# Kernel optimization log

Measured on AMD Instinct MI355X. Metric: run time of the kernel, lower is better.

The kernel has to match this reference:

```python
import jax, jax.numpy as jnp
import numpy as np

B, T, U, D, INNER, VOCAB = 4, 256, 64, 512, 512, 2048

def setup_inputs() -> dict:
    key = jax.random.key(0)
    ks = jax.random.split(key, 6)
    return {
        "enc_state": jax.random.normal(ks[0], (B, T, D), jnp.float32),
        "dec_state": jax.random.normal(ks[1], (B, U, D), jnp.float32),
        "W1": jax.random.normal(ks[2], (2 * D, INNER), jnp.float32) * 0.02,
        "b1": jax.random.normal(ks[3], (INNER,), jnp.float32) * 0.02,
        "W2": jax.random.normal(ks[4], (INNER, VOCAB), jnp.float32) * 0.02,
        "b2": jax.random.normal(ks[5], (VOCAB,), jnp.float32) * 0.02,
    }

def reference(enc_state, dec_state, W1, b1, W2, b2):
    # concat([enc, dec]) @ W1 == enc @ W1[:D] + dec @ W1[D:]  (same math,
    # avoids materializing the [B,T,U,2D] repeat+cat tensor)
    d = enc_state.shape[-1]
    We, Wd = W1[:d], W1[d:]
    enc_proj = jnp.einsum('btd,dk->btk', enc_state, We)           # [B,T,INNER]
    dec_proj = jnp.einsum('bud,dk->buk', dec_state, Wd)           # [B,U,INNER]
    hidden = jnp.tanh(enc_proj[:, :, None, :] + dec_proj[:, None, :, :] + b1)  # [B,T,U,INNER]
    logits = jnp.einsum('btuk,kv->btuv', hidden, W2) + b2          # [B,T,U,VOCAB]
    return logits
```

## Files before the change

### kernel.cpp

```cpp
#include <hip/hip_runtime.h>
#include <hip/hip_bf16.h>

#define B_  4
#define T_  256
#define U_  64
#define D_  512
#define INNER_ 512
#define VOCAB_ 2048

typedef __attribute__((ext_vector_type(8))) short short8;
typedef __attribute__((ext_vector_type(4))) float f32x4;

__global__ __launch_bounds__(256) void proj_kernel(
    const float* __restrict__ enc, const float* __restrict__ dec,
    const float* __restrict__ W1, const float* __restrict__ b1,
    float* __restrict__ encP, float* __restrict__ decPb) {
  int ct = blockIdx.x;
  int rt = blockIdx.y;
  const float* src; float* dst; int kOff; int addB1; int rowBase;
  if (rt < 64) { src = enc; dst = encP; kOff = 0; addB1 = 0; rowBase = rt * 16; }
  else { src = dec; dst = decPb; kOff = D_; addB1 = 1; rowBase = (rt - 64) * 16; }

  __shared__ float As[16][D_];
  int tid = threadIdx.x;
  const float4* s4 = (const float4*)(src + (size_t)rowBase * D_);
  float4* a4 = (float4*)(&As[0][0]);
#pragma unroll
  for (int i = 0; i < 8; i++) a4[tid + 256 * i] = s4[tid + 256 * i];
  __syncthreads();

  int colQ = (tid & 31) * 4;
  int col = ct * 128 + colQ;
  int r0 = (tid >> 5) * 2;
  float a00=0,a01=0,a02=0,a03=0, a10=0,a11=0,a12=0,a13=0;
  const float* Wp = W1 + (size_t)kOff * INNER_ + col;
#pragma unroll 4
  for (int k = 0; k < D_; k++) {
    float4 w = *(const float4*)(Wp + (size_t)k * INNER_);
    float e0 = As[r0][k], e1 = As[r0 + 1][k];
    a00 += e0 * w.x; a01 += e0 * w.y; a02 += e0 * w.z; a03 += e0 * w.w;
    a10 += e1 * w.x; a11 += e1 * w.y; a12 += e1 * w.z; a13 += e1 * w.w;
  }
  float4 bb = {0,0,0,0};
  if (addB1) bb = *(const float4*)(b1 + col);
  float4 o0 = {a00 + bb.x, a01 + bb.y, a02 + bb.z, a03 + bb.w};
  float4 o1 = {a10 + bb.x, a11 + bb.y, a12 + bb.z, a13 + bb.w};
  *(float4*)(dst + (size_t)(rowBase + r0) * INNER_ + col) = o0;
  *(float4*)(dst + (size_t)(rowBase + r0 + 1) * INNER_ + col) = o1;
}

__global__ __launch_bounds__(256) void w2t_kernel(
    const float* __restrict__ W2, __hip_bfloat16* __restrict__ W2T) {
  __shared__ float tile[32][33];
  int vBase = blockIdx.x * 32;
  int kBase = blockIdx.y * 32;
  int tx = threadIdx.x & 31, ty = threadIdx.x >> 5;
#pragma unroll
  for (int i = 0; i < 32; i += 8)
    tile[ty + i][tx] = W2[(size_t)(kBase + ty + i) * VOCAB_ + vBase + tx];
  __syncthreads();
#pragma unroll
  for (int i = 0; i < 32; i += 8)
    W2T[(size_t)(vBase + ty + i) * INNER_ + kBase + tx] = __float2bfloat16(tile[tx][ty + i]);
}

__global__ __launch_bounds__(256) void hidden_kernel(
    const float* __restrict__ encP, const float* __restrict__ decPb,
    __hip_bfloat16* __restrict__ H) {
  int gid = blockIdx.x * 256 + threadIdx.x;
  int k0 = (gid & 63) * 8;
  int r = gid >> 6;
  int u = r & 63;
  int bt = r >> 6;
  int b = bt >> 8;
  const float4* e = (const float4*)(encP + (size_t)bt * 512 + k0);
  const float4* dv = (const float4*)(decPb + (size_t)(b * 64 + u) * 512 + k0);
  float4 e0 = e[0], e1 = e[1];
  float4 d0 = dv[0], d1 = dv[1];
  union { __hip_bfloat16 h[8]; uint4 v; } p;
  p.h[0] = __float2bfloat16(tanhf(e0.x + d0.x));
  p.h[1] = __float2bfloat16(tanhf(e0.y + d0.y));
  p.h[2] = __float2bfloat16(tanhf(e0.z + d0.z));
  p.h[3] = __float2bfloat16(tanhf(e0.w + d0.w));
  p.h[4] = __float2bfloat16(tanhf(e1.x + d1.x));
  p.h[5] = __float2bfloat16(tanhf(e1.y + d1.y));
  p.h[6] = __float2bfloat16(tanhf(e1.z + d1.z));
  p.h[7] = __float2bfloat16(tanhf(e1.w + d1.w));
  *(uint4*)((__hip_bfloat16*)H + (size_t)r * 512 + k0) = p.v;
}

__device__ inline void gload_lds16(const void* g, void* l) {
  __builtin_amdgcn_global_load_lds(
      (const __attribute__((address_space(1))) unsigned int*)g,
      (__attribute__((address_space(3))) unsigned int*)l, 16, 0, 0);
}

__global__ __launch_bounds__(256, 2) void joint_gemm(
    const __hip_bfloat16* __restrict__ H, const __hip_bfloat16* __restrict__ W2T,
    const float* __restrict__ b2, float* __restrict__ out) {
  extern __shared__ char smem[];
  int tid = threadIdx.x;
  int lane = tid & 63, wave = tid >> 6;
  int wm = wave >> 1, wn = wave & 1;

  int bid = blockIdx.x;
  int wg = (bid & 7) * 512 + (bid >> 3);
  int rt = wg >> 4;
  int ct = wg & 15;
  size_t rowBase = (size_t)rt * 256;
  int colBase = ct * 128;

  int srow = tid >> 2;
  int kswz = ((tid & 3) ^ ((tid >> 3) & 3)) * 8;
  const __hip_bfloat16* pA = H   + (rowBase + srow) * 512 + kswz;
  const __hip_bfloat16* pB = W2T + (size_t)(colBase + srow) * 512 + kswz;
  char* ldsA = smem;
  char* ldsB = smem + 32768;

#define STAGE(t, buf) do {                                                    \
    const __hip_bfloat16* ga = pA + (size_t)(t) * 32;                         \
    const __hip_bfloat16* gb = pB + (size_t)(t) * 32;                         \
    char* la = ldsA + (buf) * 16384 + wave * 1024;                            \
    char* lb = ldsB + (buf) * 8192 + wave * 1024;                             \
    _Pragma("unroll")                                                         \
    for (int j = 0; j < 4; j++)                                               \
      gload_lds16(ga + (size_t)j * 64 * 512, la + j * 4096);                  \
    _Pragma("unroll")                                                         \
    for (int j = 0; j < 2; j++)                                               \
      gload_lds16(gb + (size_t)j * 64 * 512, lb + j * 4096);                  \
  } while (0)

  int laneOff = (lane & 15) * 64 + (((lane >> 4) ^ (((lane & 15) >> 1) & 3)) * 16);
  int offA = wm * 8192 + laneOff;
  int offB = wn * 4096 + laneOff;

  float bv[4];
#pragma unroll
  for (int ni = 0; ni < 4; ni++) bv[ni] = b2[colBase + wn * 64 + ni * 16 + (lane & 15)];
  f32x4 acc[8][4];
#pragma unroll
  for (int mi = 0; mi < 8; mi++)
#pragma unroll
    for (int ni = 0; ni < 4; ni++)
      acc[mi][ni] = (f32x4){bv[ni], bv[ni], bv[ni], bv[ni]};

  asm volatile("s_waitcnt vmcnt(0)" ::: "memory");
  __builtin_amdgcn_sched_barrier(0);

  STAGE(0, 0);
  STAGE(1, 1);

#define KITER(t, buf, VMC, DOSTAGE) do {                                      \
    asm volatile("s_waitcnt vmcnt(" #VMC ")" ::: "memory");                   \
    __builtin_amdgcn_sched_barrier(0);                                        \
    __builtin_amdgcn_s_barrier();                                             \
    __builtin_amdgcn_sched_barrier(0);                                        \
    const char* baA = ldsA + (buf) * 16384;                                   \
    const char* baB = ldsB + (buf) * 8192;                                    \
    short8 afr[8], bfr[4];                                                    \
    _Pragma("unroll") for (int ni = 0; ni < 4; ni++)                          \
      bfr[ni] = *(const short8*)(baB + offB + ni * 1024);                     \
    _Pragma("unroll") for (int mi = 0; mi < 8; mi++)                          \
      afr[mi] = *(const short8*)(baA + offA + mi * 1024);                     \
    asm volatile("s_waitcnt lgkmcnt(0)" ::: "memory");                        \
    __builtin_amdgcn_sched_barrier(0);                                        \
    __builtin_amdgcn_s_barrier();                                             \
    __builtin_amdgcn_sched_barrier(0);                                        \
    if (DOSTAGE) { STAGE((t) + 2, (buf)); }                                   \
    __builtin_amdgcn_sched_barrier(0);                                        \
    __builtin_amdgcn_s_setprio(1);                                            \
    _Pragma("unroll") for (int mi = 0; mi < 8; mi++)                          \
      _Pragma("unroll") for (int ni = 0; ni < 4; ni++)                        \
        acc[mi][ni] = __builtin_amdgcn_mfma_f32_16x16x32_bf16(                \
            afr[mi], bfr[ni], acc[mi][ni], 0, 0, 0);                          \
    __builtin_amdgcn_s_setprio(0);                                            \
  } while (0)

#pragma unroll 2
  for (int t = 0; t < 14; ++t) KITER(t, (t & 1), 6, 1);
  KITER(14, 0, 6, 0);
  KITER(15, 1, 0, 0);
#undef KITER
#undef STAGE

  {
    float* lp = (float*)smem;
    float* outBase = out + rowBase * VOCAB_ + colBase;
#pragma unroll
    for (int r = 0; r < 4; r++) {
      __syncthreads();
      if (wm == (r >> 1)) {
        int mih = (r & 1) * 4;
#pragma unroll
        for (int q = 0; q < 4; q++) {
          int lrow0 = q * 16 + ((lane >> 4) << 2);
#pragma unroll
          for (int ni = 0; ni < 4; ni++) {
            int col = wn * 64 + ni * 16 + (lane & 15);
            f32x4 v = acc[mih + q][ni];
#pragma unroll
            for (int j = 0; j < 4; j++)
              lp[(lrow0 + j) * 132 + col] = v[j];
          }
        }
      }
      __syncthreads();
#pragma unroll
      for (int i = 0; i < 8; i++) {
        int c = tid + 256 * i;
        int row = c >> 5, cc = c & 31;
        f32x4 v = *(const f32x4*)(lp + row * 132 + cc * 4);
        *(float4*)(outBase + (size_t)(r * 64 + row) * VOCAB_ + cc * 4) =
            (float4){v[0], v[1], v[2], v[3]};
      }
    }
  }
}

extern "C" void kernel_launch(void* const* d_in, const int* in_sizes, int n_in,
                              void* d_out, int out_size, void* d_ws, size_t ws_size,
                              hipStream_t stream) {
  const float* enc = (const float*)d_in[0];
  const float* dec = (const float*)d_in[1];
  const float* W1  = (const float*)d_in[2];
  const float* b1  = (const float*)d_in[3];
  const float* W2  = (const float*)d_in[4];
  const float* b2  = (const float*)d_in[5];
  float* out = (float*)d_out;

  char* ws = (char*)d_ws;
  float* encP  = (float*)ws;
  float* decPb = (float*)(ws + (2u << 20));
  __hip_bfloat16* W2T = (__hip_bfloat16*)(ws + (2u << 20) + (512u << 10));
  __hip_bfloat16* H   = (__hip_bfloat16*)(ws + (2u << 20) + (512u << 10) + (2u << 20));

  static int smem_set = 0;
  if (!smem_set) {
    (void)hipFuncSetAttribute((const void*)joint_gemm,
                              hipFuncAttributeMaxDynamicSharedMemorySize, 49152);
    smem_set = 1;
  }

  proj_kernel<<<dim3(4, 80), 256, 0, stream>>>(enc, dec, W1, b1, encP, decPb);
  w2t_kernel<<<dim3(64, 16), 256, 0, stream>>>(W2, W2T);
  hidden_kernel<<<16384, 256, 0, stream>>>(encP, decPb, H);
  joint_gemm<<<dim3(4096), 256, 49152, stream>>>(H, W2T, b2, out);
}
```

Before: 728.9 us.

## Widen GEMM tile to 256x256 with 8 waves, merge prep kernels, nontemporal stores

```diff
diff --git a/kernel.cpp b/kernel.cpp
--- a/kernel.cpp
+++ b/kernel.cpp
@@ -11,57 +11,62 @@
 typedef __attribute__((ext_vector_type(8))) short short8;
 typedef __attribute__((ext_vector_type(4))) float f32x4;
 
-__global__ __launch_bounds__(256) void proj_kernel(
+__global__ __launch_bounds__(256) void prep_kernel(
     const float* __restrict__ enc, const float* __restrict__ dec,
     const float* __restrict__ W1, const float* __restrict__ b1,
-    float* __restrict__ encP, float* __restrict__ decPb) {
-  int ct = blockIdx.x;
-  int rt = blockIdx.y;
-  const float* src; float* dst; int kOff; int addB1; int rowBase;
-  if (rt < 64) { src = enc; dst = encP; kOff = 0; addB1 = 0; rowBase = rt * 16; }
-  else { src = dec; dst = decPb; kOff = D_; addB1 = 1; rowBase = (rt - 64) * 16; }
-
-  __shared__ float As[16][D_];
+    const float* __restrict__ W2,
+    float* __restrict__ encP, float* __restrict__ decPb,
+    __hip_bfloat16* __restrict__ W2T) {
+  __shared__ float ldsbuf[16 * D_];
   int tid = threadIdx.x;
-  const float4* s4 = (const float4*)(src + (size_t)rowBase * D_);
-  float4* a4 = (float4*)(&As[0][0]);
-#pragma unroll
-  for (int i = 0; i < 8; i++) a4[tid + 256 * i] = s4[tid + 256 * i];
-  __syncthreads();
-
-  int colQ = (tid & 31) * 4;
-  int col = ct * 128 + colQ;
-  int r0 = (tid >> 5) * 2;
-  float a00=0,a01=0,a02=0,a03=0, a10=0,a11=0,a12=0,a13=0;
-  const float* Wp = W1 + (size_t)kOff * INNER_ + col;
+  int bidx = blockIdx.x;
+
+  if (bidx < 320) {
+    int ct = bidx & 3;
+    int rt = bidx >> 2;
+    const float* src; float* dst; int kOff; int addB1; int rowBase;
+    if (rt < 64) { src = enc; dst = encP; kOff = 0; addB1 = 0; rowBase = rt * 16; }
+    else { src = dec; dst = decPb; kOff = D_; addB1 = 1; rowBase = (rt - 64) * 16; }
+
+    float (*As)[D_] = (float(*)[D_])ldsbuf;
+    const float4* s4 = (const float4*)(src + (size_t)rowBase * D_);
+    float4* a4 = (float4*)(&As[0][0]);
+#pragma unroll
+    for (int i = 0; i < 8; i++) a4[tid + 256 * i] = s4[tid + 256 * i];
+    __syncthreads();
+
+    int colQ = (tid & 31) * 4;
+    int col = ct * 128 + colQ;
+    int r0 = (tid >> 5) * 2;
+    float a00=0,a01=0,a02=0,a03=0, a10=0,a11=0,a12=0,a13=0;
+    const float* Wp = W1 + (size_t)kOff * INNER_ + col;
 #pragma unroll 4
-  for (int k = 0; k < D_; k++) {
-    float4 w = *(const float4*)(Wp + (size_t)k * INNER_);
-    float e0 = As[r0][k], e1 = As[r0 + 1][k];
-    a00 += e0 * w.x; a01 += e0 * w.y; a02 += e0 * w.z; a03 += e0 * w.w;
-    a10 += e1 * w.x; a11 += e1 * w.y; a12 += e1 * w.z; a13 += e1 * w.w;
+    for (int k = 0; k < D_; k++) {
+      float4 w = *(const float4*)(Wp + (size_t)k * INNER_);
+      float e0 = As[r0][k], e1 = As[r0 + 1][k];
+      a00 += e0 * w.x; a01 += e0 * w.y; a02 += e0 * w.z; a03 += e0 * w.w;
+      a10 += e1 * w.x; a11 += e1 * w.y; a12 += e1 * w.z; a13 += e1 * w.w;
+    }
+    float4 bb = {0,0,0,0};
+    if (addB1) bb = *(const float4*)(b1 + col);
+    float4 o0 = {a00 + bb.x, a01 + bb.y, a02 + bb.z, a03 + bb.w};
+    float4 o1 = {a10 + bb.x, a11 + bb.y, a12 + bb.z, a13 + bb.w};
+    *(float4*)(dst + (size_t)(rowBase + r0) * INNER_ + col) = o0;
+    *(float4*)(dst + (size_t)(rowBase + r0 + 1) * INNER_ + col) = o1;
+  } else {
+    int b = bidx - 320;
+    int vBase = (b & 63) * 32;
+    int kBase = (b >> 6) * 32;
+    float (*tile)[33] = (float(*)[33])ldsbuf;
+    int tx = tid & 31, ty = tid >> 5;
+#pragma unroll
+    for (int i = 0; i < 32; i += 8)
+      tile[ty + i][tx] = W2[(size_t)(kBase + ty + i) * VOCAB_ + vBase + tx];
+    __syncthreads();
+#pragma unroll
+    for (int i = 0; i < 32; i += 8)
+      W2T[(size_t)(vBase + ty + i) * INNER_ + kBase + tx] = __float2bfloat16(tile[tx][ty + i]);
   }
-  float4 bb = {0,0,0,0};
-  if (addB1) bb = *(const float4*)(b1 + col);
-  float4 o0 = {a00 + bb.x, a01 + bb.y, a02 + bb.z, a03 + bb.w};
-  float4 o1 = {a10 + bb.x, a11 + bb.y, a12 + bb.z, a13 + bb.w};
-  *(float4*)(dst + (size_t)(rowBase + r0) * INNER_ + col) = o0;
-  *(float4*)(dst + (size_t)(rowBase + r0 + 1) * INNER_ + col) = o1;
-}
-
-__global__ __launch_bounds__(256) void w2t_kernel(
-    const float* __restrict__ W2, __hip_bfloat16* __restrict__ W2T) {
-  __shared__ float tile[32][33];
-  int vBase = blockIdx.x * 32;
-  int kBase = blockIdx.y * 32;
-  int tx = threadIdx.x & 31, ty = threadIdx.x >> 5;
-#pragma unroll
-  for (int i = 0; i < 32; i += 8)
-    tile[ty + i][tx] = W2[(size_t)(kBase + ty + i) * VOCAB_ + vBase + tx];
-  __syncthreads();
-#pragma unroll
-  for (int i = 0; i < 32; i += 8)
-    W2T[(size_t)(vBase + ty + i) * INNER_ + kBase + tx] = __float2bfloat16(tile[tx][ty + i]);
 }
 
 __global__ __launch_bounds__(256) void hidden_kernel(
@@ -95,23 +100,23 @@
       (__attribute__((address_space(3))) unsigned int*)l, 16, 0, 0);
 }
 
-__global__ __launch_bounds__(256, 2) void joint_gemm(
+__global__ __launch_bounds__(512, 1) void joint_gemm(
     const __hip_bfloat16* __restrict__ H, const __hip_bfloat16* __restrict__ W2T,
     const float* __restrict__ b2, float* __restrict__ out) {
   extern __shared__ char smem[];
   int tid = threadIdx.x;
   int lane = tid & 63, wave = tid >> 6;
-  int wm = wave >> 1, wn = wave & 1;
+  int wm = wave >> 2, wn = wave & 3;
 
   int bid = blockIdx.x;
-  int wg = (bid & 7) * 512 + (bid >> 3);
-  int rt = wg >> 4;
-  int ct = wg & 15;
+  int wg = (bid & 7) * 256 + (bid >> 3);
+  int rt = wg >> 3;
+  int ct = wg & 7;
   size_t rowBase = (size_t)rt * 256;
-  int colBase = ct * 128;
-
-  int srow = tid >> 2;
-  int kswz = ((tid & 3) ^ ((tid >> 3) & 3)) * 8;
+  int colBase = ct * 256;
+
+  int kswz = ((lane & 3) ^ ((lane >> 3) & 3)) * 8;
+  int srow = wave * 16 + (lane >> 2);
   const __hip_bfloat16* pA = H   + (rowBase + srow) * 512 + kswz;
   const __hip_bfloat16* pB = W2T + (size_t)(colBase + srow) * 512 + kswz;
   char* ldsA = smem;
@@ -121,13 +126,11 @@
     const __hip_bfloat16* ga = pA + (size_t)(t) * 32;                         \
     const __hip_bfloat16* gb = pB + (size_t)(t) * 32;                         \
     char* la = ldsA + (buf) * 16384 + wave * 1024;                            \
-    char* lb = ldsB + (buf) * 8192 + wave * 1024;                             \
-    _Pragma("unroll")                                                         \
-    for (int j = 0; j < 4; j++)                                               \
-      gload_lds16(ga + (size_t)j * 64 * 512, la + j * 4096);                  \
-    _Pragma("unroll")                                                         \
-    for (int j = 0; j < 2; j++)                                               \
-      gload_lds16(gb + (size_t)j * 64 * 512, lb + j * 4096);                  \
+    char* lb = ldsB + (buf) * 16384 + wave * 1024;                            \
+    gload_lds16(ga,                 la);                                      \
+    gload_lds16(ga + 128 * 512,     la + 8192);                               \
+    gload_lds16(gb,                 lb);                                      \
+    gload_lds16(gb + 128 * 512,     lb + 8192);                               \
   } while (0)
 
   int laneOff = (lane & 15) * 64 + (((lane >> 4) ^ (((lane & 15) >> 1) & 3)) * 16);
@@ -156,7 +159,7 @@
     __builtin_amdgcn_s_barrier();                                             \
     __builtin_amdgcn_sched_barrier(0);                                        \
     const char* baA = ldsA + (buf) * 16384;                                   \
-    const char* baB = ldsB + (buf) * 8192;                                    \
+    const char* baB = ldsB + (buf) * 16384;                                   \
     short8 afr[8], bfr[4];                                                    \
     _Pragma("unroll") for (int ni = 0; ni < 4; ni++)                          \
       bfr[ni] = *(const short8*)(baB + offB + ni * 1024);                     \
@@ -177,8 +180,8 @@
   } while (0)
 
 #pragma unroll 2
-  for (int t = 0; t < 14; ++t) KITER(t, (t & 1), 6, 1);
-  KITER(14, 0, 6, 0);
+  for (int t = 0; t < 14; ++t) KITER(t, (t & 1), 4, 1);
+  KITER(14, 0, 4, 0);
   KITER(15, 1, 0, 0);
 #undef KITER
 #undef STAGE
@@ -200,18 +203,18 @@
             f32x4 v = acc[mih + q][ni];
 #pragma unroll
             for (int j = 0; j < 4; j++)
-              lp[(lrow0 + j) * 132 + col] = v[j];
+              lp[(lrow0 + j) * 260 + col] = v[j];
           }
         }
       }
       __syncthreads();
 #pragma unroll
       for (int i = 0; i < 8; i++) {
-        int c = tid + 256 * i;
-        int row = c >> 5, cc = c & 31;
-        f32x4 v = *(const f32x4*)(lp + row * 132 + cc * 4);
-        *(float4*)(outBase + (size_t)(r * 64 + row) * VOCAB_ + cc * 4) =
-            (float4){v[0], v[1], v[2], v[3]};
+        int c = tid + 512 * i;
+        int row = c >> 6, cc = c & 63;
+        f32x4 v = *(const f32x4*)(lp + row * 260 + cc * 4);
+        __builtin_nontemporal_store(
+            v, (f32x4*)(outBase + (size_t)(r * 64 + row) * VOCAB_ + cc * 4));
       }
     }
   }
@@ -237,12 +240,11 @@
   static int smem_set = 0;
   if (!smem_set) {
     (void)hipFuncSetAttribute((const void*)joint_gemm,
-                              hipFuncAttributeMaxDynamicSharedMemorySize, 49152);
+                              hipFuncAttributeMaxDynamicSharedMemorySize, 66560);
     smem_set = 1;
   }
 
-  proj_kernel<<<dim3(4, 80), 256, 0, stream>>>(enc, dec, W1, b1, encP, decPb);
-  w2t_kernel<<<dim3(64, 16), 256, 0, stream>>>(W2, W2T);
+  prep_kernel<<<dim3(1344), 256, 0, stream>>>(enc, dec, W1, b1, W2, encP, decPb, W2T);
   hidden_kernel<<<16384, 256, 0, stream>>>(encP, decPb, H);
-  joint_gemm<<<dim3(4096), 256, 49152, stream>>>(H, W2T, b2, out);
-}
+  joint_gemm<<<dim3(2048), 512, 66560, stream>>>(H, W2T, b2, out);
+}
```

Result: faster. 697.2 us (-4.4%).
